# Kernel optimization log

Hardware: AMD Instinct MI355X
Metric: run time of the kernel (lower is better)

The kernel has to match this reference:

```python
import jax, jax.numpy as jnp
import numpy as np

B, S, DIM = 2, 2048, 4096
HQ, HKV, HD = 32, 8, 128
N_REP = HQ // HKV
MAX_S = 2048
ROPE_BASE = 10000.0


def rotate_half(x):
    half = x.shape[-1] // 2
    return jnp.concatenate([-x[..., half:], x[..., :half]], axis=-1)


def setup_inputs() -> dict:
    key = jax.random.key(0)
    ks = jax.random.split(key, 8)
    x = jax.random.normal(ks[0], (B, S, DIM), dtype=jnp.float32)
    Wq = jax.random.normal(ks[1], (HQ * HD, DIM), dtype=jnp.float32) * 0.02
    bq = jax.random.normal(ks[2], (HQ * HD,), dtype=jnp.float32) * 0.02
    Wk = jax.random.normal(ks[3], (HKV * HD, DIM), dtype=jnp.float32) * 0.02
    bk = jax.random.normal(ks[4], (HKV * HD,), dtype=jnp.float32) * 0.02
    Wv = jax.random.normal(ks[5], (HKV * HD, DIM), dtype=jnp.float32) * 0.02
    bv = jax.random.normal(ks[6], (HKV * HD,), dtype=jnp.float32) * 0.02
    Wo = jax.random.normal(ks[7], (DIM, HQ * HD), dtype=jnp.float32) * 0.02
    # RoPE tables (HF convention: angles duplicated across both halves)
    inv_freq = 1.0 / (ROPE_BASE ** (jnp.arange(0, HD, 2, dtype=jnp.float32) / HD))
    pos = jnp.arange(S, dtype=jnp.float32)
    ang = pos[:, None] * inv_freq[None, :]              # [S, HD/2]
    emb = jnp.concatenate([ang, ang], axis=-1)          # [S, HD]
    cos, sin = jnp.cos(emb), jnp.sin(emb)
    # static KV cache, zero-initialized as in the module
    cache_k = jnp.zeros((B, HKV, MAX_S, HD), dtype=jnp.float32)
    cache_v = jnp.zeros((B, HKV, MAX_S, HD), dtype=jnp.float32)
    # causal additive mask
    causal = jnp.tril(jnp.ones((S, S), dtype=bool))
    mask = jnp.where(causal, 0.0, -1e9).astype(jnp.float32)[None, None]  # [1,1,S,S]
    return {"x": x, "cos": cos, "sin": sin, "Wq": Wq, "bq": bq, "Wk": Wk,
            "bk": bk, "Wv": Wv, "bv": bv, "Wo": Wo, "cache_k": cache_k,
            "cache_v": cache_v, "mask": mask, "start_pos": 0}


def reference(x, cos, sin, Wq, bq, Wk, bk, Wv, bv, Wo, cache_k, cache_v, mask, start_pos):
    bsz, seqlen, _ = x.shape
    scaling = 1.0 / jnp.sqrt(jnp.float32(HD))
    # QKV projections
    xq = (jnp.einsum('bsd,ed->bse', x, Wq) + bq).reshape(bsz, seqlen, HQ, HD).transpose(0, 2, 1, 3)
    xk = (jnp.einsum('bsd,ed->bse', x, Wk) + bk).reshape(bsz, seqlen, HKV, HD).transpose(0, 2, 1, 3)
    xv = (jnp.einsum('bsd,ed->bse', x, Wv) + bv).reshape(bsz, seqlen, HKV, HD).transpose(0, 2, 1, 3)
    # RoPE
    c = cos[None, None]  # [1,1,S,HD]
    s = sin[None, None]
    xq = xq * c + rotate_half(xq) * s
    xk = xk * c + rotate_half(xk) * s
    # static KV-cache append + slice (start_pos is a Python int)
    cache_k = jax.lax.dynamic_update_slice(cache_k, xk, (0, 0, start_pos, 0))
    cache_v = jax.lax.dynamic_update_slice(cache_v, xv, (0, 0, start_pos, 0))
    keys = cache_k[:, :, :start_pos + seqlen]     # [B,HKV,K,HD]
    values = cache_v[:, :, :start_pos + seqlen]
    # GQA: repeat kv heads (repeat_interleave over head dim)
    keys = jnp.repeat(keys, N_REP, axis=1)        # [B,HQ,K,HD]
    values = jnp.repeat(values, N_REP, axis=1)
    # SDPA with additive mask
    scores = jnp.einsum('bhqd,bhkd->bhqk', xq, keys) * scaling + mask
    attn = jax.nn.softmax(scores, axis=-1)
    out = jnp.einsum('bhqk,bhkd->bhqd', attn, values)
    out = out.transpose(0, 2, 1, 3).reshape(bsz, seqlen, HQ * HD)
    return jnp.einsum('bse,de->bsd', out, Wo)
```

## Files before the change

kernel.cpp:

```cpp
#include <hip/hip_runtime.h>

typedef _Float16 half8 __attribute__((ext_vector_type(8)));
typedef _Float16 half4 __attribute__((ext_vector_type(4)));
typedef _Float16 half2v __attribute__((ext_vector_type(2)));
typedef float floatx4 __attribute__((ext_vector_type(4)));
typedef float floatx16 __attribute__((ext_vector_type(16)));

#define SWZ(r) ((((r) & 7) << 1) | (((r) >> 3) & 1))

__device__ __forceinline__ void gld16(const void* g, void* l) {
  __builtin_amdgcn_global_load_lds(
      (const __attribute__((address_space(1))) unsigned int*)g,
      (__attribute__((address_space(3))) unsigned int*)l, 16, 0, 0);
}

__global__ void convert_all(const float* __restrict__ x, const float* __restrict__ Wq,
                            const float* __restrict__ Wk, const float* __restrict__ Wv,
                            const float* __restrict__ Wo, const float* __restrict__ bq,
                            const float* __restrict__ bk, const float* __restrict__ bv,
                            _Float16* __restrict__ xb, _Float16* __restrict__ wqkv,
                            _Float16* __restrict__ wo_b, float* __restrict__ biasc) {
  long i = (long)blockIdx.x * 256 + threadIdx.x;
  const long N0 = 2097152, N1 = N0 + 2097152, N2 = N1 + 524288, N3 = N2 + 524288,
             N4 = N3 + 2097152;
  const float* s;
  _Float16* d;
  long j;
  if (i < N0) { s = x; d = xb; j = i; }
  else if (i < N1) { s = Wq; d = wqkv; j = i - N0; }
  else if (i < N2) { s = Wk; d = wqkv + (size_t)4096 * 4096; j = i - N1; }
  else if (i < N3) { s = Wv; d = wqkv + (size_t)5120 * 4096; j = i - N2; }
  else if (i < N4) { s = Wo; d = wo_b; j = i - N3; }
  else {
    long k = i - N4;
    if (k < 4096) biasc[k] = bq[k];
    else if (k < 5120) biasc[k] = bk[k - 4096];
    else if (k < 6144) biasc[k] = bv[k - 5120];
    return;
  }
  float4 a = ((const float4*)s)[2 * j];
  float4 b2 = ((const float4*)s)[2 * j + 1];
  half8 h;
  h[0] = (_Float16)a.x; h[1] = (_Float16)a.y; h[2] = (_Float16)a.z; h[3] = (_Float16)a.w;
  h[4] = (_Float16)b2.x; h[5] = (_Float16)b2.y; h[6] = (_Float16)b2.z; h[7] = (_Float16)b2.w;
  ((half8*)d)[j] = h;
}

__global__ __launch_bounds__(256) void gemm_qkv_fused(
    const _Float16* __restrict__ A, const _Float16* __restrict__ B,
    const float* __restrict__ bias, const float* __restrict__ cosb,
    const float* __restrict__ sinb, _Float16* __restrict__ q_r,
    _Float16* __restrict__ k_r, _Float16* __restrict__ v_t, int hoff, int M, int K) {
  __shared__ _Float16 smem[128 * 130];
  _Float16* as = smem;
  _Float16* bs = smem + 128 * 64;
  const int tid = threadIdx.x;
  const int w = tid >> 6, lane = tid & 63;
  const int quad = lane >> 4, l16 = lane & 15;
  const int hh = hoff + blockIdx.x;
  const int M0 = blockIdx.y * 128, N0 = hh * 128;
  const int wm = (w >> 1) * 64, wn = (w & 1) * 64;

  floatx4 acc[4][4];
#pragma unroll
  for (int i = 0; i < 4; ++i)
#pragma unroll
    for (int j = 0; j < 4; ++j) acc[i][j] = (floatx4){0.f, 0.f, 0.f, 0.f};

  const int sr = tid >> 3, g0 = tid & 7;
  const int csw = (g0 ^ (sr & 7)) * 8;
  const _Float16* Ag[4];
  const _Float16* Bg[4];
  _Float16* asd[4];
  _Float16* bsd[4];
#pragma unroll
  for (int c = 0; c < 4; ++c) {
    Ag[c] = A + (size_t)(M0 + c * 32 + sr) * K + csw;
    Bg[c] = B + (size_t)(N0 + c * 32 + sr) * K + csw;
    asd[c] = &as[(c * 32 + w * 8) * 64];
    bsd[c] = &bs[(c * 32 + w * 8) * 64];
  }

  int aoff[4][2], boff[4][2];
#pragma unroll
  for (int mi = 0; mi < 4; ++mi)
#pragma unroll
    for (int kd = 0; kd < 2; ++kd) {
      int ra = wm + mi * 16 + l16;
      aoff[mi][kd] = ra * 64 + (((kd * 4 + quad) ^ (ra & 7)) * 8);
      int rb = wn + mi * 16 + l16;
      boff[mi][kd] = rb * 64 + (((kd * 4 + quad) ^ (rb & 7)) * 8);
    }

  for (int kk = 0; kk < K; kk += 64) {
    __syncthreads();
#pragma unroll
    for (int c = 0; c < 4; ++c) gld16(Ag[c] + kk, asd[c]);
#pragma unroll
    for (int c = 0; c < 4; ++c) gld16(Bg[c] + kk, bsd[c]);
    __syncthreads();
#pragma unroll
    for (int kd = 0; kd < 2; ++kd) {
      half8 af[4], bf[4];
#pragma unroll
      for (int i = 0; i < 4; ++i) af[i] = *(const half8*)&as[aoff[i][kd]];
#pragma unroll
      for (int i = 0; i < 4; ++i) bf[i] = *(const half8*)&bs[boff[i][kd]];
#pragma unroll
      for (int mi = 0; mi < 4; ++mi)
#pragma unroll
        for (int ni = 0; ni < 4; ++ni)
          acc[mi][ni] = __builtin_amdgcn_mfma_f32_16x16x32_f16(af[mi], bf[ni], acc[mi][ni], 0, 0, 0);
    }
  }

  __syncthreads();
#pragma unroll
  for (int mi = 0; mi < 4; ++mi)
#pragma unroll
    for (int ni = 0; ni < 4; ++ni) {
      int col = wn + ni * 16 + l16;
      float bvv = bias[N0 + col];
#pragma unroll
      for (int r = 0; r < 4; ++r) {
        int row = wm + mi * 16 + quad * 4 + r;
        smem[row * 130 + col] = (_Float16)(acc[mi][ni][r] + bvv);
      }
    }
  __syncthreads();

  const int bb = M0 >> 11;
  const int sl0 = M0 & 2047;

  if (hh < 40) {
    _Float16* base = (hh < 32)
        ? q_r + ((size_t)(bb * 32 + hh) * 2048 + sl0) * 128
        : k_r + ((size_t)(bb * 8 + (hh - 32)) * 2048 + sl0) * 128;
    const float sc = (hh < 32) ? 0.12751744737079736f : 1.0f;
    const int d4 = (tid & 15) * 4, r0 = tid >> 4;
#pragma unroll
    for (int pp = 0; pp < 8; ++pp) {
      int row = r0 + pp * 16;
      int sl = sl0 + row;
      float4 cc = *(const float4*)&cosb[sl * 128 + d4];
      float4 ss = *(const float4*)&sinb[sl * 128 + d4];
      half4 x1 = *(const half4*)&smem[row * 130 + d4];
      half4 x2 = *(const half4*)&smem[row * 130 + d4 + 64];
      const float* cf = (const float*)&cc;
      const float* sf = (const float*)&ss;
      half4 o1, o2;
#pragma unroll
      for (int i = 0; i < 4; ++i) {
        float xx1 = (float)x1[i], xx2 = (float)x2[i];
        o1[i] = (_Float16)((xx1 * cf[i] - xx2 * sf[i]) * sc);
        o2[i] = (_Float16)((xx2 * cf[i] + xx1 * sf[i]) * sc);
      }
      *(half4*)&base[(size_t)row * 128 + d4] = o1;
      *(half4*)&base[(size_t)row * 128 + d4 + 64] = o2;
    }
  } else {
    const int hv = hh - 40;
    _Float16* vb = v_t + (size_t)(bb * 8 + hv) * 128 * 2048 + sl0;
    const int d0 = tid >> 6, sp = (tid & 63) * 2;
#pragma unroll
    for (int pp = 0; pp < 32; ++pp) {
      int d = d0 + pp * 4;
      half2v o;
      o[0] = smem[sp * 130 + d];
      o[1] = smem[(sp + 1) * 130 + d];
      *(half2v*)&vb[(size_t)d * 2048 + sp] = o;
    }
  }
}

template <typename OutT, bool HasBias>
__global__ __launch_bounds__(512, 2) void gemm256(const _Float16* __restrict__ A,
                                                  const _Float16* __restrict__ B,
                                                  const float* __restrict__ bias,
                                                  OutT* __restrict__ C, int M, int N, int K) {
  __shared__ _Float16 as[2][256 * 64];
  __shared__ _Float16 bs[2][256 * 64];
  const int tid = threadIdx.x;
  const int w = tid >> 6, lane = tid & 63;
  const int quad = lane >> 4, l16 = lane & 15;
  const int sw7 = l16 & 7;
  const int M0 = blockIdx.y * 256, N0 = blockIdx.x * 256;
  const int wm = (w >> 2) * 128, wn = (w & 3) * 64;
  const int NT = K >> 6;

  floatx4 acc[8][4];
#pragma unroll
  for (int i = 0; i < 8; ++i)
#pragma unroll
    for (int j = 0; j < 4; ++j) acc[i][j] = (floatx4){0.f, 0.f, 0.f, 0.f};

  const int sr = tid >> 3;
  const int csw = ((tid & 7) ^ (sr & 7)) * 8;
  const _Float16* Ag[4];
  const _Float16* Bg[4];
#pragma unroll
  for (int j = 0; j < 4; ++j) {
    Ag[j] = A + (size_t)(M0 + j * 64 + sr) * K + csw;
    Bg[j] = B + (size_t)(N0 + j * 64 + sr) * K + csw;
  }

#define STA(p, t, j) gld16(Ag[j] + (size_t)(t) * 64, &as[p][(j) * 4096 + w * 512])
#define STB(p, t, j) gld16(Bg[j] + (size_t)(t) * 64, &bs[p][(j) * 4096 + w * 512])

#define FRA(p, q, mi, kd) \
  (*(const half8*)&as[p][(wm + (q) * 32 + (mi) * 16 + l16) * 64 + ((((kd) * 4 + quad) ^ sw7) * 8)])
#define FRB(p, ni, kd) \
  (*(const half8*)&bs[p][(wn + (ni) * 16 + l16) * 64 + ((((kd) * 4 + quad) ^ sw7) * 8)])

#define LD_A(p, q)                                   \
  _Pragma("unroll") for (int kd = 0; kd < 2; ++kd)   \
  _Pragma("unroll") for (int mi = 0; mi < 2; ++mi)   \
      af[mi][kd] = FRA(p, q, mi, kd);

#define LD_B(p)                                      \
  _Pragma("unroll") for (int kd = 0; kd < 2; ++kd)   \
  _Pragma("unroll") for (int ni = 0; ni < 4; ++ni)   \
      bf[ni][kd] = FRB(p, ni, kd);

#define PH_COMPUTE(q)                                                                  \
  __builtin_amdgcn_s_barrier();                                                        \
  asm volatile("s_waitcnt lgkmcnt(0)" ::: "memory");                                   \
  __builtin_amdgcn_sched_barrier(0);                                                   \
  __builtin_amdgcn_s_setprio(1);                                                       \
  _Pragma("unroll") for (int kd = 0; kd < 2; ++kd)                                     \
  _Pragma("unroll") for (int mi = 0; mi < 2; ++mi)                                     \
  _Pragma("unroll") for (int ni = 0; ni < 4; ++ni)                                     \
      acc[(q) * 2 + mi][ni] = __builtin_amdgcn_mfma_f32_16x16x32_f16(                  \
          af[mi][kd], bf[ni][kd], acc[(q) * 2 + mi][ni], 0, 0, 0);                     \
  __builtin_amdgcn_s_setprio(0);

  half8 bf[4][2], af[2][2];

  STA(0, 0, 0); STA(0, 0, 1); STA(0, 0, 2); STA(0, 0, 3);
  STB(0, 0, 0); STB(0, 0, 1); STB(0, 0, 2); STB(0, 0, 3);
  STB(1, 1, 0); STB(1, 1, 1); STB(1, 1, 2); STB(1, 1, 3);
  asm volatile("s_waitcnt vmcnt(4)" ::: "memory");
  __builtin_amdgcn_s_barrier();

  for (int t = 0; t < NT; t += 2) {
    const int t2 = (t + 2 < NT) ? t + 2 : t;
    const int t3 = (t + 3 < NT) ? t + 3 : t + 1;

    LD_B(0); LD_A(0, 0);
    STA(1, t + 1, 0); STA(1, t + 1, 1); STA(1, t + 1, 2); STA(1, t + 1, 3);
    PH_COMPUTE(0);
    __builtin_amdgcn_s_barrier();

    LD_A(0, 1);
    STB(0, t2, 0); STB(0, t2, 1);
    PH_COMPUTE(1);
    __builtin_amdgcn_s_barrier();

    LD_A(0, 2);
    STB(0, t2, 2); STB(0, t2, 3);
    PH_COMPUTE(2);
    __builtin_amdgcn_s_barrier();

    LD_A(0, 3);
    PH_COMPUTE(3);
    asm volatile("s_waitcnt vmcnt(4)" ::: "memory");
    __builtin_amdgcn_sched_barrier(0);
    __builtin_amdgcn_s_barrier();

    LD_B(1); LD_A(1, 0);
    STA(0, t2, 0); STA(0, t2, 1);
    PH_COMPUTE(0);
    __builtin_amdgcn_s_barrier();

    LD_A(1, 1);
    STA(0, t2, 2); STA(0, t2, 3);
    PH_COMPUTE(1);
    __builtin_amdgcn_s_barrier();

    LD_A(1, 2);
    STB(1, t3, 0); STB(1, t3, 1);
    PH_COMPUTE(2);
    __builtin_amdgcn_s_barrier();

    LD_A(1, 3);
    STB(1, t3, 2); STB(1, t3, 3);
    PH_COMPUTE(3);
    asm volatile("s_waitcnt vmcnt(4)" ::: "memory");
    __builtin_amdgcn_sched_barrier(0);
    __builtin_amdgcn_s_barrier();
  }
  asm volatile("s_waitcnt vmcnt(0)" ::: "memory");

#pragma unroll
  for (int mf = 0; mf < 8; ++mf)
#pragma unroll
    for (int ni = 0; ni < 4; ++ni) {
      int row = M0 + wm + mf * 16 + quad * 4;
      int col = N0 + wn + ni * 16 + l16;
      float bvv = HasBias ? bias[col] : 0.f;
#pragma unroll
      for (int r = 0; r < 4; ++r) C[(size_t)(row + r) * N + col] = (OutT)(acc[mf][ni][r] + bvv);
    }
#undef STA
#undef STB
#undef FRA
#undef FRB
#undef LD_A
#undef LD_B
#undef PH_COMPUTE
}

__global__ __launch_bounds__(256, 2) void attn_kernel(const _Float16* __restrict__ q_r,
                                                      const _Float16* __restrict__ k_r,
                                                      const _Float16* __restrict__ v_t,
                                                      _Float16* __restrict__ att) {
  __shared__ __align__(16) _Float16 kbuf[2][64 * 128];
  __shared__ __align__(16) _Float16 vbuf[2][128 * 64];
  const int tid = threadIdx.x;
  const int w = tid >> 6, lane = tid & 63;
  const int l32 = lane & 31, hi = lane >> 5;
  const int qb = 15 - blockIdx.x;
  const int h = blockIdx.y, b = blockIdx.z;
  const int q0 = qb * 128;
  const _Float16* qh = q_r + ((size_t)(b * 32 + h) * 2048) * 128;
  const _Float16* kh = k_r + ((size_t)(b * 8 + (h >> 2)) * 2048) * 128;
  const _Float16* vh = v_t + ((size_t)(b * 8 + (h >> 2)) * 128) * 2048;

  const int ql = w * 32 + l32;
  const int myq = q0 + ql;
  const int swq7 = ql & 7;
  const int swl = SWZ(l32);

  half8 bq[8];
#pragma unroll
  for (int kd = 0; kd < 8; ++kd)
    bq[kd] = *(const half8*)&qh[(size_t)myq * 128 + kd * 16 + hi * 8];

  floatx16 oacc[4];
#pragma unroll
  for (int di = 0; di < 4; ++di)
#pragma unroll
    for (int j = 0; j < 16; ++j) oacc[di][j] = 0.f;
  float mrun = -1e30f, lrun = 0.f;

  const int krow = tid >> 4, kgrp = tid & 15;
  const int vrow = tid >> 3, vgrp = tid & 7;

#define STAGE_KV(p, t)                                                                     \
  do {                                                                                     \
    const _Float16* kg_ = kh + (size_t)(t) * 64 * 128;                                     \
    _Pragma("unroll") for (int c = 0; c < 4; ++c) {                                        \
      int row = c * 16 + krow;                                                             \
      gld16(kg_ + row * 128 + ((kgrp ^ SWZ(row)) * 8), &kbuf[p][(c * 16 + w * 4) * 128]);  \
    }                                                                                      \
    _Pragma("unroll") for (int c = 0; c < 4; ++c) {                                        \
      int row = c * 32 + vrow;                                                             \
      gld16(vh + (size_t)row * 2048 + (size_t)(t) * 64 + ((vgrp ^ (row & 7)) * 8),         \
            &vbuf[p][(c * 32 + w * 8) * 64]);                                              \
    }                                                                                      \
  } while (0)

  const int nsteps = 2 * qb + 2;
  STAGE_KV(0, 0);

  for (int s = 0; s < nsteps; ++s) {
    const int cur = s & 1;
    __syncthreads();
    const int sn = (s + 1 < nsteps) ? s + 1 : s;
    STAGE_KV(cur ^ 1, sn);
    asm volatile("s_waitcnt vmcnt(8)" ::: "memory");
    __syncthreads();

    floatx16 sacc[2];
#pragma unroll
    for (int ni = 0; ni < 2; ++ni)
#pragma unroll
      for (int j = 0; j < 16; ++j) sacc[ni][j] = 0.f;
#pragma unroll
    for (int ni = 0; ni < 2; ++ni) {
      int rb = (ni * 32 + l32) * 128;
#pragma unroll
      for (int kd = 0; kd < 8; ++kd) {
        half8 ka = *(const half8*)&kbuf[cur][rb + (((kd * 2 + hi) ^ swl) * 8)];
        sacc[ni] = __builtin_amdgcn_mfma_f32_32x32x16_f16(ka, bq[kd], sacc[ni], 0, 0, 0);
      }
    }

    if (s >= 2 * qb) {
      int kv0 = s * 64;
#pragma unroll
      for (int ni = 0; ni < 2; ++ni)
#pragma unroll
        for (int g = 0; g < 4; ++g) {
          int kvb = kv0 + ni * 32 + g * 8 + hi * 4;
#pragma unroll
          for (int t = 0; t < 4; ++t)
            if (kvb + t > myq) sacc[ni][g * 4 + t] = -1e30f;
        }
    }

    float tm = -1e30f;
#pragma unroll
    for (int ni = 0; ni < 2; ++ni)
#pragma unroll
      for (int j = 0; j < 16; ++j) tm = fmaxf(tm, sacc[ni][j]);
    tm = fmaxf(tm, __shfl_xor(tm, 32));
    float nm = fmaxf(mrun, tm);
    float al = exp2f(mrun - nm);
    mrun = nm;
    float ts = 0.f;
#pragma unroll
    for (int ni = 0; ni < 2; ++ni)
#pragma unroll
      for (int j = 0; j < 16; ++j) {
        float p = exp2f(sacc[ni][j] - nm);
        sacc[ni][j] = p;
        ts += p;
      }
    ts += __shfl_xor(ts, 32);
    lrun = lrun * al + ts;
#pragma unroll
    for (int di = 0; di < 4; ++di)
#pragma unroll
      for (int j = 0; j < 16; ++j) oacc[di][j] *= al;

    __syncthreads();

#pragma unroll
    for (int ni = 0; ni < 2; ++ni)
#pragma unroll
      for (int g = 0; g < 4; ++g) {
        half4 p4;
#pragma unroll
        for (int t = 0; t < 4; ++t) p4[t] = (_Float16)sacc[ni][g * 4 + t];
        *(half4*)&kbuf[cur][ql * 64 + (((ni * 4 + g) ^ swq7) * 8) + hi * 4] = p4;
      }

#pragma unroll
    for (int ks = 0; ks < 4; ++ks) {
      half8 pb = *(const half8*)&kbuf[cur][ql * 64 + (((ks * 2 + hi) ^ swq7) * 8)];
#pragma unroll
      for (int di = 0; di < 4; ++di) {
        int rv = (di * 32 + l32) * 64;
        half8 va = *(const half8*)&vbuf[cur][rv + (((ks * 2 + hi) ^ (l32 & 7)) * 8)];
        oacc[di] = __builtin_amdgcn_mfma_f32_32x32x16_f16(va, pb, oacc[di], 0, 0, 0);
      }
    }
  }
  asm volatile("s_waitcnt vmcnt(0)" ::: "memory");

  float inv = 1.f / lrun;
  _Float16* ob = att + ((size_t)b * 2048 + myq) * 4096 + h * 128;
#pragma unroll
  for (int di = 0; di < 4; ++di)
#pragma unroll
    for (int g = 0; g < 4; ++g) {
      half4 o4;
#pragma unroll
      for (int t = 0; t < 4; ++t) o4[t] = (_Float16)(oacc[di][g * 4 + t] * inv);
      *(half4*)&ob[di * 32 + g * 8 + hi * 4] = o4;
    }
#undef STAGE_KV
}

extern "C" void kernel_launch(void* const* d_in, const int* in_sizes, int n_in, void* d_out,
                              int out_size, void* d_ws, size_t ws_size, hipStream_t stream) {
  const float* x = (const float*)d_in[0];
  const float* cosb = (const float*)d_in[1];
  const float* sinb = (const float*)d_in[2];
  const float* Wq = (const float*)d_in[3];
  const float* bq = (const float*)d_in[4];
  const float* Wk = (const float*)d_in[5];
  const float* bk = (const float*)d_in[6];
  const float* Wv = (const float*)d_in[7];
  const float* bv = (const float*)d_in[8];
  const float* Wo = (const float*)d_in[9];
  float* out = (float*)d_out;

  char* p = (char*)d_ws;
  _Float16* xb = (_Float16*)p;   p += (size_t)4096 * 4096 * 2;
  _Float16* wqkv = (_Float16*)p; p += (size_t)6144 * 4096 * 2;
  _Float16* wo_b = (_Float16*)p; p += (size_t)4096 * 4096 * 2;
  _Float16* q_r = (_Float16*)p;  p += (size_t)2 * 32 * 2048 * 128 * 2;
  _Float16* k_r = (_Float16*)p;  p += (size_t)2 * 8 * 2048 * 128 * 2;
  _Float16* v_t = (_Float16*)p;  p += (size_t)2 * 8 * 128 * 2048 * 2;
  _Float16* att = (_Float16*)p;  p += (size_t)4096 * 4096 * 2;
  float* biasc = (float*)p;      p += 6144 * 4;

  convert_all<<<28696, 256, 0, stream>>>(x, Wq, Wk, Wv, Wo, bq, bk, bv, xb, wqkv, wo_b, biasc);

  gemm_qkv_fused<<<dim3(32, 32), 256, 0, stream>>>(xb, wqkv, biasc, cosb, sinb, q_r, k_r, v_t,
                                                   0, 4096, 4096);
  gemm_qkv_fused<<<dim3(16, 32), 256, 0, stream>>>(xb, wqkv, biasc, cosb, sinb, q_r, k_r, v_t,
                                                   32, 4096, 4096);
  attn_kernel<<<dim3(16, 32, 2), 256, 0, stream>>>(q_r, k_r, v_t, att);
  gemm256<float, false><<<dim3(16, 16), 512, 0, stream>>>(att, wo_b, nullptr, out, 4096, 4096, 4096);
}
```

Measured before the change: 886.3 us.

## Single-buffer attention K/V with separate P buffer, raise occupancy, merge QKV launches

```diff
diff --git a/kernel.cpp b/kernel.cpp
--- a/kernel.cpp
+++ b/kernel.cpp
@@ -310,12 +310,13 @@
 #undef PH_COMPUTE
 }
 
-__global__ __launch_bounds__(256, 2) void attn_kernel(const _Float16* __restrict__ q_r,
+__global__ __launch_bounds__(256, 3) void attn_kernel(const _Float16* __restrict__ q_r,
                                                       const _Float16* __restrict__ k_r,
                                                       const _Float16* __restrict__ v_t,
                                                       _Float16* __restrict__ att) {
-  __shared__ __align__(16) _Float16 kbuf[2][64 * 128];
-  __shared__ __align__(16) _Float16 vbuf[2][128 * 64];
+  __shared__ __align__(16) _Float16 kbuf[64 * 128];
+  __shared__ __align__(16) _Float16 vbuf[128 * 64];
+  __shared__ __align__(16) _Float16 pbuf[128 * 64];
   const int tid = threadIdx.x;
   const int w = tid >> 6, lane = tid & 63;
   const int l32 = lane & 31, hi = lane >> 5;
@@ -346,29 +347,25 @@
   const int krow = tid >> 4, kgrp = tid & 15;
   const int vrow = tid >> 3, vgrp = tid & 7;
 
-#define STAGE_KV(p, t)                                                                     \
-  do {                                                                                     \
-    const _Float16* kg_ = kh + (size_t)(t) * 64 * 128;                                     \
-    _Pragma("unroll") for (int c = 0; c < 4; ++c) {                                        \
-      int row = c * 16 + krow;                                                             \
-      gld16(kg_ + row * 128 + ((kgrp ^ SWZ(row)) * 8), &kbuf[p][(c * 16 + w * 4) * 128]);  \
-    }                                                                                      \
-    _Pragma("unroll") for (int c = 0; c < 4; ++c) {                                        \
-      int row = c * 32 + vrow;                                                             \
-      gld16(vh + (size_t)row * 2048 + (size_t)(t) * 64 + ((vgrp ^ (row & 7)) * 8),         \
-            &vbuf[p][(c * 32 + w * 8) * 64]);                                              \
-    }                                                                                      \
-  } while (0)
-
   const int nsteps = 2 * qb + 2;
-  STAGE_KV(0, 0);
 
   for (int s = 0; s < nsteps; ++s) {
-    const int cur = s & 1;
     __syncthreads();
-    const int sn = (s + 1 < nsteps) ? s + 1 : s;
-    STAGE_KV(cur ^ 1, sn);
-    asm volatile("s_waitcnt vmcnt(8)" ::: "memory");
+    {
+      const _Float16* kg_ = kh + (size_t)s * 64 * 128;
+#pragma unroll
+      for (int c = 0; c < 4; ++c) {
+        int row = c * 16 + krow;
+        gld16(kg_ + row * 128 + ((kgrp ^ SWZ(row)) * 8), &kbuf[(c * 16 + w * 4) * 128]);
+      }
+#pragma unroll
+      for (int c = 0; c < 4; ++c) {
+        int row = c * 32 + vrow;
+        gld16(vh + (size_t)row * 2048 + (size_t)s * 64 + ((vgrp ^ (row & 7)) * 8),
+              &vbuf[(c * 32 + w * 8) * 64]);
+      }
+    }
+    asm volatile("s_waitcnt vmcnt(0)" ::: "memory");
     __syncthreads();
 
     floatx16 sacc[2];
@@ -376,15 +373,17 @@
     for (int ni = 0; ni < 2; ++ni)
 #pragma unroll
       for (int j = 0; j < 16; ++j) sacc[ni][j] = 0.f;
+    __builtin_amdgcn_s_setprio(1);
 #pragma unroll
     for (int ni = 0; ni < 2; ++ni) {
       int rb = (ni * 32 + l32) * 128;
 #pragma unroll
       for (int kd = 0; kd < 8; ++kd) {
-        half8 ka = *(const half8*)&kbuf[cur][rb + (((kd * 2 + hi) ^ swl) * 8)];
+        half8 ka = *(const half8*)&kbuf[rb + (((kd * 2 + hi) ^ swl) * 8)];
         sacc[ni] = __builtin_amdgcn_mfma_f32_32x32x16_f16(ka, bq[kd], sacc[ni], 0, 0, 0);
       }
     }
+    __builtin_amdgcn_s_setprio(0);
 
     if (s >= 2 * qb) {
       int kv0 = s * 64;
@@ -424,8 +423,6 @@
 #pragma unroll
       for (int j = 0; j < 16; ++j) oacc[di][j] *= al;
 
-    __syncthreads();
-
 #pragma unroll
     for (int ni = 0; ni < 2; ++ni)
 #pragma unroll
@@ -433,21 +430,22 @@
         half4 p4;
 #pragma unroll
         for (int t = 0; t < 4; ++t) p4[t] = (_Float16)sacc[ni][g * 4 + t];
-        *(half4*)&kbuf[cur][ql * 64 + (((ni * 4 + g) ^ swq7) * 8) + hi * 4] = p4;
-      }
-
+        *(half4*)&pbuf[ql * 64 + (((ni * 4 + g) ^ swq7) * 8) + hi * 4] = p4;
+      }
+
+    __builtin_amdgcn_s_setprio(1);
 #pragma unroll
     for (int ks = 0; ks < 4; ++ks) {
-      half8 pb = *(const half8*)&kbuf[cur][ql * 64 + (((ks * 2 + hi) ^ swq7) * 8)];
+      half8 pb = *(const half8*)&pbuf[ql * 64 + (((ks * 2 + hi) ^ swq7) * 8)];
 #pragma unroll
       for (int di = 0; di < 4; ++di) {
         int rv = (di * 32 + l32) * 64;
-        half8 va = *(const half8*)&vbuf[cur][rv + (((ks * 2 + hi) ^ (l32 & 7)) * 8)];
+        half8 va = *(const half8*)&vbuf[rv + (((ks * 2 + hi) ^ (l32 & 7)) * 8)];
         oacc[di] = __builtin_amdgcn_mfma_f32_32x32x16_f16(va, pb, oacc[di], 0, 0, 0);
       }
     }
-  }
-  asm volatile("s_waitcnt vmcnt(0)" ::: "memory");
+    __builtin_amdgcn_s_setprio(0);
+  }
 
   float inv = 1.f / lrun;
   _Float16* ob = att + ((size_t)b * 2048 + myq) * 4096 + h * 128;
@@ -460,7 +458,6 @@
       for (int t = 0; t < 4; ++t) o4[t] = (_Float16)(oacc[di][g * 4 + t] * inv);
       *(half4*)&ob[di * 32 + g * 8 + hi * 4] = o4;
     }
-#undef STAGE_KV
 }
 
 extern "C" void kernel_launch(void* const* d_in, const int* in_sizes, int n_in, void* d_out,
@@ -484,15 +481,13 @@
   _Float16* q_r = (_Float16*)p;  p += (size_t)2 * 32 * 2048 * 128 * 2;
   _Float16* k_r = (_Float16*)p;  p += (size_t)2 * 8 * 2048 * 128 * 2;
   _Float16* v_t = (_Float16*)p;  p += (size_t)2 * 8 * 128 * 2048 * 2;
-  _Float16* att = (_Float16*)p;  p += (size_t)4096 * 4096 * 2;
   float* biasc = (float*)p;      p += 6144 * 4;
+  _Float16* att = xb;
 
   convert_all<<<28696, 256, 0, stream>>>(x, Wq, Wk, Wv, Wo, bq, bk, bv, xb, wqkv, wo_b, biasc);
 
-  gemm_qkv_fused<<<dim3(32, 32), 256, 0, stream>>>(xb, wqkv, biasc, cosb, sinb, q_r, k_r, v_t,
+  gemm_qkv_fused<<<dim3(48, 32), 256, 0, stream>>>(xb, wqkv, biasc, cosb, sinb, q_r, k_r, v_t,
                                                    0, 4096, 4096);
-  gemm_qkv_fused<<<dim3(16, 32), 256, 0, stream>>>(xb, wqkv, biasc, cosb, sinb, q_r, k_r, v_t,
-                                                   32, 4096, 4096);
   attn_kernel<<<dim3(16, 32, 2), 256, 0, stream>>>(q_r, k_r, v_t, att);
   gemm256<float, false><<<dim3(16, 16), 512, 0, stream>>>(att, wo_b, nullptr, out, 4096, 4096, 4096);
 }
```

Result: faster. 851.2 us (-4.0%).
